# Kernel optimization log

Measured on AMD Instinct MI355X. Metric: run time of the kernel, lower is better.

## Reference

```python
import jax, jax.numpy as jnp
import numpy as np

D_MODEL = 1024
NUM_HEADS = 16
HEAD_DIM = D_MODEL // NUM_HEADS


def setup_inputs() -> dict:
    key = jax.random.key(0)
    ks = jax.random.split(key, 9)
    s = 1.0 / np.sqrt(D_MODEL)
    x = jax.random.normal(ks[0], (2, 2048, D_MODEL), dtype=jnp.float32)
    Wq = jax.random.normal(ks[1], (D_MODEL, D_MODEL), dtype=jnp.float32) * s
    Wk = jax.random.normal(ks[2], (D_MODEL, D_MODEL), dtype=jnp.float32) * s
    Wv = jax.random.normal(ks[3], (D_MODEL, D_MODEL), dtype=jnp.float32) * s
    Wo = jax.random.normal(ks[4], (D_MODEL, D_MODEL), dtype=jnp.float32) * s
    bq = jax.random.normal(ks[5], (D_MODEL,), dtype=jnp.float32) * s
    bk = jax.random.normal(ks[6], (D_MODEL,), dtype=jnp.float32) * s
    bv = jax.random.normal(ks[7], (D_MODEL,), dtype=jnp.float32) * s
    bo = jax.random.normal(ks[8], (D_MODEL,), dtype=jnp.float32) * s
    return {"x": x, "Wq": Wq, "bq": bq, "Wk": Wk, "bk": bk, "Wv": Wv, "bv": bv, "Wo": Wo, "bo": bo}


def reference(x, Wq, bq, Wk, bk, Wv, bv, Wo, bo):
    B, S, D = x.shape
    H, Hd = NUM_HEADS, HEAD_DIM
    # QKV projections
    q = (x @ Wq + bq).reshape(B, S, H, Hd).transpose(0, 2, 1, 3)  # [B,H,S,Hd]
    k = (x @ Wk + bk).reshape(B, S, H, Hd).transpose(0, 2, 1, 3)
    v = (x @ Wv + bv).reshape(B, S, H, Hd).transpose(0, 2, 1, 3)
    scores = jnp.einsum("bhqd,bhkd->bhqk", q, k) / jnp.sqrt(jnp.float32(Hd))
    attn = jax.nn.softmax(scores, axis=-1)
    out = jnp.einsum("bhqk,bhkd->bhqd", attn, v)  # [B,H,S,Hd]
    out = out.transpose(0, 2, 1, 3).reshape(B, S, D)
    return out @ Wo + bo
```

## Files before the change

kernel.cpp:

```cpp
#include <hip/hip_runtime.h>
#include <hip/hip_bf16.h>


typedef unsigned short u16;

#define D_MODEL 1024
#define NHEAD 16
#define HDIM 64
#define BATCH 2
#define SEQ 2048
#define MTOT (BATCH * SEQ)

#define QSCALE 0.18033688011112042f

using frag_ab = __attribute__((ext_vector_type(8))) short;
using frag_cd = __attribute__((ext_vector_type(4))) float;

__device__ __forceinline__ u16 f2u(float f) {
    union { float f; unsigned int i; } x;
    x.f = f;
    unsigned int r = x.i + 0x7fffu + ((x.i >> 16) & 1u);
    return (u16)(r >> 16);
}
__device__ __forceinline__ u16 f2u_fast(float f) {
    union { float f; unsigned int i; } x;
    x.f = f;
    return (u16)((x.i + 0x8000u) >> 16);
}

__global__ void prep(const float* __restrict__ W0, const float* __restrict__ W1,
                     const float* __restrict__ W2, const float* __restrict__ W3,
                     const float* __restrict__ X, u16* __restrict__ Wt,
                     u16* __restrict__ Xb) {
    const int z = blockIdx.z;
    const int tx = threadIdx.x, ty = threadIdx.y;
    if (z < 4) {
        __shared__ u16 t[32][33];
        const float* W = (z == 0) ? W0 : (z == 1) ? W1 : (z == 2) ? W2 : W3;
        u16* o = Wt + (size_t)z * D_MODEL * D_MODEL;
        int n0 = blockIdx.x * 32, k0 = blockIdx.y * 32;
        #pragma unroll
        for (int i = ty; i < 32; i += 8) t[i][tx] = f2u(W[(size_t)(k0 + i) * D_MODEL + n0 + tx]);
        __syncthreads();
        #pragma unroll
        for (int i = ty; i < 32; i += 8) o[(size_t)(n0 + i) * D_MODEL + k0 + tx] = t[tx][i];
    } else {
        int tid = ty * 32 + tx;
        size_t base = ((size_t)(blockIdx.y * 32 + blockIdx.x) * 256 + tid) * 16;
        #pragma unroll
        for (int c = 0; c < 4; ++c) {
            float4 v = *(const float4*)&X[base + c * 4];
            ushort4 o;
            o.x = f2u(v.x); o.y = f2u(v.y); o.z = f2u(v.z); o.w = f2u(v.w);
            *(ushort4*)&Xb[base + c * 4] = o;
        }
    }
}

__launch_bounds__(256, 2)
__global__ void gemm_qkvt(const u16* __restrict__ xb, const u16* __restrict__ Wt,
                          const float* __restrict__ bq, const float* __restrict__ bk,
                          const float* __restrict__ bv, u16* __restrict__ QKw,
                          u16* __restrict__ Vtw) {
    constexpr int BK = 64;
    __shared__ __attribute__((aligned(16))) u16 As[128 * BK];
    __shared__ __attribute__((aligned(16))) u16 Bs[128 * BK];

    const int tid = threadIdx.x;
    const int w = tid >> 6;
    const int lane = tid & 63;
    const int lrow = lane & 15, lquad = lane >> 4;
    const size_t WSZ = (size_t)D_MODEL * D_MODEL;

    const int bid = blockIdx.x;
    const bool vt = bid >= 512;
    const int z = vt ? 2 : (bid >> 8);
    const int t = vt ? (bid - 512) : (bid & 255);
    const int n0 = vt ? (t & 31) * 128 : (t & 7) * 128;
    const int m0 = vt ? (t >> 5) * 128 : (t >> 3) * 128;
    const u16* Ap = vt ? (Wt + 2 * WSZ) : xb;
    const u16* Bp = vt ? xb : (Wt + (size_t)z * WSZ);
    const float* bias = vt ? bv : (z ? bk : bq);

    frag_cd acc[4][4];
    #pragma unroll
    for (int i = 0; i < 4; i++)
        #pragma unroll
        for (int j = 0; j < 4; j++) acc[i][j] = (frag_cd){0.f, 0.f, 0.f, 0.f};

    const int wm = (w >> 1) * 64, wn = (w & 1) * 64;

    for (int k0 = 0; k0 < D_MODEL; k0 += BK) {
        __syncthreads();
        #pragma unroll
        for (int it = 0; it < 4; ++it) {
            int c = it * 256 + tid;
            int r = c >> 3, c8 = c & 7;
            const u16* ga = Ap + (size_t)(m0 + r) * D_MODEL + k0 + c8 * 8;
            char* la = (char*)As + (it * 256 + w * 64) * 16;
            __builtin_amdgcn_global_load_lds((const __attribute__((address_space(1))) void*)ga,
                                             (__attribute__((address_space(3))) void*)la, 16, 0, 0);
            const u16* gb = Bp + (size_t)(n0 + r) * D_MODEL + k0 + c8 * 8;
            char* lb = (char*)Bs + (it * 256 + w * 64) * 16;
            __builtin_amdgcn_global_load_lds((const __attribute__((address_space(1))) void*)gb,
                                             (__attribute__((address_space(3))) void*)lb, 16, 0, 0);
        }
        __syncthreads();

        #pragma unroll
        for (int kc = 0; kc < 2; ++kc) {
            frag_ab av[4], bvv[4];
            #pragma unroll
            for (int i = 0; i < 4; i++)
                av[i] = *(const frag_ab*)&As[(wm + i * 16 + lrow) * BK + kc * 32 + lquad * 8];
            #pragma unroll
            for (int j = 0; j < 4; j++)
                bvv[j] = *(const frag_ab*)&Bs[(wn + j * 16 + lrow) * BK + kc * 32 + lquad * 8];
            #pragma unroll
            for (int i = 0; i < 4; i++)
                #pragma unroll
                for (int j = 0; j < 4; j++)
                    acc[i][j] = __builtin_amdgcn_mfma_f32_16x16x32_bf16(av[i], bvv[j], acc[i][j], 0, 0, 0);
        }
    }

    const float scale = (!vt && z == 0) ? QSCALE : 1.0f;
    #pragma unroll
    for (int j = 0; j < 4; j++) {
        int gn = n0 + wn + j * 16 + lrow;
        #pragma unroll
        for (int i = 0; i < 4; i++) {
            #pragma unroll
            for (int rr = 0; rr < 4; ++rr) {
                int gm = m0 + wm + i * 16 + lquad * 4 + rr;
                if (!vt) {
                    float v = (acc[i][j][rr] + bias[gn]) * scale;
                    u16* oz = QKw + (size_t)z * ((size_t)MTOT * D_MODEL);
                    int b = gm >> 11, s = gm & (SEQ - 1);
                    int h = gn >> 6, d = gn & (HDIM - 1);
                    oz[(((size_t)(b * NHEAD + h)) * SEQ + s) * HDIM + d] = f2u(v);
                } else {
                    float v = acc[i][j][rr] + bias[gm];
                    int h = gm >> 6, d = gm & (HDIM - 1);
                    int b = gn >> 11, s = gn & (SEQ - 1);
                    Vtw[(((size_t)(b * NHEAD + h)) * HDIM + d) * SEQ + s] = f2u(v);
                }
            }
        }
    }
}

__launch_bounds__(256, 2)
__global__ void gemm_out(const u16* __restrict__ A, const u16* __restrict__ Wt,
                         const float* __restrict__ bias, float* __restrict__ out) {
    constexpr int BK = 64;
    __shared__ __attribute__((aligned(16))) u16 As[64 * BK];
    __shared__ __attribute__((aligned(16))) u16 Bs[128 * BK];

    const int tid = threadIdx.x;
    const int w = tid >> 6;
    const int lane = tid & 63;
    const int lrow = lane & 15, lquad = lane >> 4;
    const int m0 = blockIdx.y * 64, n0 = blockIdx.x * 128;

    frag_cd acc[2][4];
    #pragma unroll
    for (int i = 0; i < 2; i++)
        #pragma unroll
        for (int j = 0; j < 4; j++) acc[i][j] = (frag_cd){0.f, 0.f, 0.f, 0.f};

    const int wm = (w >> 1) * 32, wn = (w & 1) * 64;

    for (int k0 = 0; k0 < D_MODEL; k0 += BK) {
        __syncthreads();
        #pragma unroll
        for (int it = 0; it < 2; ++it) {
            int c = it * 256 + tid;
            int r = c >> 3, c8 = c & 7;
            const u16* ga = A + (size_t)(m0 + r) * D_MODEL + k0 + c8 * 8;
            char* la = (char*)As + (it * 256 + w * 64) * 16;
            __builtin_amdgcn_global_load_lds((const __attribute__((address_space(1))) void*)ga,
                                             (__attribute__((address_space(3))) void*)la, 16, 0, 0);
        }
        #pragma unroll
        for (int it = 0; it < 4; ++it) {
            int c = it * 256 + tid;
            int r = c >> 3, c8 = c & 7;
            const u16* gb = Wt + (size_t)(n0 + r) * D_MODEL + k0 + c8 * 8;
            char* lb = (char*)Bs + (it * 256 + w * 64) * 16;
            __builtin_amdgcn_global_load_lds((const __attribute__((address_space(1))) void*)gb,
                                             (__attribute__((address_space(3))) void*)lb, 16, 0, 0);
        }
        __syncthreads();

        #pragma unroll
        for (int kc = 0; kc < 2; ++kc) {
            frag_ab av[2], bvv[4];
            #pragma unroll
            for (int i = 0; i < 2; i++)
                av[i] = *(const frag_ab*)&As[(wm + i * 16 + lrow) * BK + kc * 32 + lquad * 8];
            #pragma unroll
            for (int j = 0; j < 4; j++)
                bvv[j] = *(const frag_ab*)&Bs[(wn + j * 16 + lrow) * BK + kc * 32 + lquad * 8];
            #pragma unroll
            for (int i = 0; i < 2; i++)
                #pragma unroll
                for (int j = 0; j < 4; j++)
                    acc[i][j] = __builtin_amdgcn_mfma_f32_16x16x32_bf16(av[i], bvv[j], acc[i][j], 0, 0, 0);
        }
    }

    #pragma unroll
    for (int j = 0; j < 4; j++) {
        int gn = n0 + wn + j * 16 + lrow;
        float bvf = bias[gn];
        #pragma unroll
        for (int i = 0; i < 2; i++)
            #pragma unroll
            for (int rr = 0; rr < 4; ++rr) {
                int gm = m0 + wm + i * 16 + lquad * 4 + rr;
                out[(size_t)gm * D_MODEL + gn] = acc[i][j][rr] + bvf;
            }
    }
}

__launch_bounds__(256, 2)
__global__ void attn_kernel(const u16* __restrict__ Q, const u16* __restrict__ K,
                            const u16* __restrict__ Vt, u16* __restrict__ O) {
    constexpr int SKK = 72;
    constexpr int SKV = 136;
    __shared__ __attribute__((aligned(16))) u16 Ks[128 * SKK];
    __shared__ __attribute__((aligned(16))) u16 Vs[64 * SKV];
    __shared__ __attribute__((aligned(16))) u16 Ps[4 * 32 * SKV];

    const int tid = threadIdx.x;
    const int w = tid >> 6;
    const int lane = tid & 63;
    const int lrow = lane & 15, lquad = lane >> 4;
    const int bh = blockIdx.y;
    const int q0 = blockIdx.x * 128;
    const size_t base = (size_t)bh * SEQ * HDIM;
    const u16* Qg = Q + base;
    const u16* Kg = K + base;
    const u16* Vg = Vt + base;

    frag_ab qf[2][2];
    #pragma unroll
    for (int sub = 0; sub < 2; ++sub)
        #pragma unroll
        for (int kc = 0; kc < 2; ++kc)
            qf[sub][kc] = *(const frag_ab*)&Qg[(size_t)(q0 + w * 32 + sub * 16 + lrow) * HDIM + kc * 32 + lquad * 8];

    frag_cd accO[2][4], lacc[2];
    #pragma unroll
    for (int sub = 0; sub < 2; ++sub) {
        lacc[sub] = (frag_cd){0.f, 0.f, 0.f, 0.f};
        #pragma unroll
        for (int df = 0; df < 4; df++) accO[sub][df] = (frag_cd){0.f, 0.f, 0.f, 0.f};
    }
    frag_ab ones;
    #pragma unroll
    for (int t = 0; t < 8; ++t) ones[t] = (short)0x3F80;

    u16* Pw = Ps + w * 32 * SKV;

    for (int kt = 0; kt < SEQ / 128; ++kt) {
        __syncthreads();
        #pragma unroll
        for (int it = 0; it < 4; ++it) {
            int c = it * 256 + tid;
            int rk = c >> 3, ck = (c & 7) * 8;
            *(uint4*)&Ks[rk * SKK + ck] = *(const uint4*)&Kg[(size_t)(kt * 128 + rk) * HDIM + ck];
            int rv = c >> 4, cv = (c & 15) * 8;
            *(uint4*)&Vs[rv * SKV + cv] = *(const uint4*)&Vg[(size_t)rv * SEQ + kt * 128 + cv];
        }
        __syncthreads();

        frag_cd sc[2][8];
        #pragma unroll
        for (int sub = 0; sub < 2; ++sub)
            #pragma unroll
            for (int nf = 0; nf < 8; nf++) sc[sub][nf] = (frag_cd){0.f, 0.f, 0.f, 0.f};
        #pragma unroll
        for (int kc = 0; kc < 2; ++kc) {
            #pragma unroll
            for (int nf = 0; nf < 8; nf++) {
                frag_ab kf = *(const frag_ab*)&Ks[(nf * 16 + lrow) * SKK + kc * 32 + lquad * 8];
                #pragma unroll
                for (int sub = 0; sub < 2; ++sub)
                    sc[sub][nf] = __builtin_amdgcn_mfma_f32_16x16x32_bf16(qf[sub][kc], kf, sc[sub][nf], 0, 0, 0);
            }
        }

        #pragma unroll
        for (int sub = 0; sub < 2; ++sub)
            #pragma unroll
            for (int nf = 0; nf < 8; nf++)
                #pragma unroll
                for (int i = 0; i < 4; i++)
                    Pw[(sub * 16 + lquad * 4 + i) * SKV + nf * 16 + lrow] = f2u_fast(exp2f(sc[sub][nf][i]));

        #pragma unroll
        for (int kc = 0; kc < 4; ++kc) {
            frag_ab pf[2];
            #pragma unroll
            for (int sub = 0; sub < 2; ++sub)
                pf[sub] = *(const frag_ab*)&Pw[(sub * 16 + lrow) * SKV + kc * 32 + lquad * 8];
            #pragma unroll
            for (int sub = 0; sub < 2; ++sub)
                lacc[sub] = __builtin_amdgcn_mfma_f32_16x16x32_bf16(pf[sub], ones, lacc[sub], 0, 0, 0);
            #pragma unroll
            for (int df = 0; df < 4; df++) {
                frag_ab vf = *(const frag_ab*)&Vs[(df * 16 + lrow) * SKV + kc * 32 + lquad * 8];
                #pragma unroll
                for (int sub = 0; sub < 2; ++sub)
                    accO[sub][df] = __builtin_amdgcn_mfma_f32_16x16x32_bf16(pf[sub], vf, accO[sub][df], 0, 0, 0);
            }
        }
    }

    const int b = bh >> 4, h = bh & (NHEAD - 1);
    #pragma unroll
    for (int sub = 0; sub < 2; ++sub)
        #pragma unroll
        for (int df = 0; df < 4; df++)
            #pragma unroll
            for (int i = 0; i < 4; i++) {
                int s = q0 + w * 32 + sub * 16 + lquad * 4 + i;
                int d = df * 16 + lrow;
                O[((size_t)(b * SEQ + s)) * D_MODEL + h * HDIM + d] = f2u(accO[sub][df][i] / lacc[sub][i]);
            }
}

extern "C" void kernel_launch(void* const* d_in, const int* in_sizes, int n_in,
                              void* d_out, int out_size, void* d_ws, size_t ws_size,
                              hipStream_t stream) {
    const float* x  = (const float*)d_in[0];
    const float* Wq = (const float*)d_in[1];
    const float* bq = (const float*)d_in[2];
    const float* Wk = (const float*)d_in[3];
    const float* bk = (const float*)d_in[4];
    const float* Wv = (const float*)d_in[5];
    const float* bv = (const float*)d_in[6];
    const float* Wo = (const float*)d_in[7];
    const float* bo = (const float*)d_in[8];

    u16* ws = (u16*)d_ws;
    const size_t WSZ = (size_t)D_MODEL * D_MODEL;
    const size_t TSZ = (size_t)MTOT * D_MODEL;
    u16* xb  = ws;
    u16* Wt  = ws + 4 * WSZ;
    u16* QKw = ws + 8 * WSZ;
    u16* Vtw = QKw + 2 * TSZ;
    u16* Aw  = Vtw + TSZ;

    prep<<<dim3(32, 32, 5), dim3(32, 8), 0, stream>>>(Wq, Wk, Wv, Wo, x, Wt, xb);
    gemm_qkvt<<<dim3(768), 256, 0, stream>>>(xb, Wt, bq, bk, bv, QKw, Vtw);
    attn_kernel<<<dim3(16, 32), 256, 0, stream>>>(QKw, QKw + TSZ, Vtw, Aw);
    gemm_out<<<dim3(8, 64), 256, 0, stream>>>(Aw, Wt + 3 * WSZ, bo, (float*)d_out);
}
```

Before: 223.6 us.

## Use 8 waves of 16 query rows each in attention and raise occupancy bounds

The attention kernel moves from 4 waves each handling 32 query rows to 8 waves each handling 16 rows, with 512 threads per block. This halves per-wave register state and spreads the cooperative K/V tile loads across more threads. The intent is more latency hiding through higher occupancy. The cost is that each K and V fragment read from shared memory now feeds half as many MFMAs, adding LDS traffic per unit of work. The QKV GEMM's launch bound is also raised to 3 blocks per CU, which may force register spills.

```diff
diff --git a/kernel.cpp b/kernel.cpp
--- a/kernel.cpp
+++ b/kernel.cpp
@@ -57,7 +57,7 @@
     }
 }
 
-__launch_bounds__(256, 2)
+__launch_bounds__(256, 3)
 __global__ void gemm_qkvt(const u16* __restrict__ xb, const u16* __restrict__ Wt,
                           const float* __restrict__ bq, const float* __restrict__ bk,
                           const float* __restrict__ bv, u16* __restrict__ QKw,
@@ -224,14 +224,14 @@
     }
 }
 
-__launch_bounds__(256, 2)
+__launch_bounds__(512, 4)
 __global__ void attn_kernel(const u16* __restrict__ Q, const u16* __restrict__ K,
                             const u16* __restrict__ Vt, u16* __restrict__ O) {
     constexpr int SKK = 72;
     constexpr int SKV = 136;
     __shared__ __attribute__((aligned(16))) u16 Ks[128 * SKK];
     __shared__ __attribute__((aligned(16))) u16 Vs[64 * SKV];
-    __shared__ __attribute__((aligned(16))) u16 Ps[4 * 32 * SKV];
+    __shared__ __attribute__((aligned(16))) u16 Ps[8 * 16 * SKV];
 
     const int tid = threadIdx.x;
     const int w = tid >> 6;
@@ -244,31 +244,26 @@
     const u16* Kg = K + base;
     const u16* Vg = Vt + base;
 
-    frag_ab qf[2][2];
-    #pragma unroll
-    for (int sub = 0; sub < 2; ++sub)
-        #pragma unroll
-        for (int kc = 0; kc < 2; ++kc)
-            qf[sub][kc] = *(const frag_ab*)&Qg[(size_t)(q0 + w * 32 + sub * 16 + lrow) * HDIM + kc * 32 + lquad * 8];
-
-    frag_cd accO[2][4], lacc[2];
-    #pragma unroll
-    for (int sub = 0; sub < 2; ++sub) {
-        lacc[sub] = (frag_cd){0.f, 0.f, 0.f, 0.f};
-        #pragma unroll
-        for (int df = 0; df < 4; df++) accO[sub][df] = (frag_cd){0.f, 0.f, 0.f, 0.f};
-    }
+    frag_ab qf[2];
+    #pragma unroll
+    for (int kc = 0; kc < 2; ++kc)
+        qf[kc] = *(const frag_ab*)&Qg[(size_t)(q0 + w * 16 + lrow) * HDIM + kc * 32 + lquad * 8];
+
+    frag_cd accO[4], lacc;
+    lacc = (frag_cd){0.f, 0.f, 0.f, 0.f};
+    #pragma unroll
+    for (int df = 0; df < 4; df++) accO[df] = (frag_cd){0.f, 0.f, 0.f, 0.f};
     frag_ab ones;
     #pragma unroll
     for (int t = 0; t < 8; ++t) ones[t] = (short)0x3F80;
 
-    u16* Pw = Ps + w * 32 * SKV;
+    u16* Pw = Ps + w * 16 * SKV;
 
     for (int kt = 0; kt < SEQ / 128; ++kt) {
         __syncthreads();
         #pragma unroll
-        for (int it = 0; it < 4; ++it) {
-            int c = it * 256 + tid;
+        for (int it = 0; it < 2; ++it) {
+            int c = it * 512 + tid;
             int rk = c >> 3, ck = (c & 7) * 8;
             *(uint4*)&Ks[rk * SKK + ck] = *(const uint4*)&Kg[(size_t)(kt * 128 + rk) * HDIM + ck];
             int rv = c >> 4, cv = (c & 15) * 8;
@@ -276,60 +271,45 @@
         }
         __syncthreads();
 
-        frag_cd sc[2][8];
-        #pragma unroll
-        for (int sub = 0; sub < 2; ++sub)
-            #pragma unroll
-            for (int nf = 0; nf < 8; nf++) sc[sub][nf] = (frag_cd){0.f, 0.f, 0.f, 0.f};
+        frag_cd sc[8];
+        #pragma unroll
+        for (int nf = 0; nf < 8; nf++) sc[nf] = (frag_cd){0.f, 0.f, 0.f, 0.f};
         #pragma unroll
         for (int kc = 0; kc < 2; ++kc) {
             #pragma unroll
             for (int nf = 0; nf < 8; nf++) {
                 frag_ab kf = *(const frag_ab*)&Ks[(nf * 16 + lrow) * SKK + kc * 32 + lquad * 8];
-                #pragma unroll
-                for (int sub = 0; sub < 2; ++sub)
-                    sc[sub][nf] = __builtin_amdgcn_mfma_f32_16x16x32_bf16(qf[sub][kc], kf, sc[sub][nf], 0, 0, 0);
+                sc[nf] = __builtin_amdgcn_mfma_f32_16x16x32_bf16(qf[kc], kf, sc[nf], 0, 0, 0);
             }
         }
 
         #pragma unroll
-        for (int sub = 0; sub < 2; ++sub)
-            #pragma unroll
-            for (int nf = 0; nf < 8; nf++)
-                #pragma unroll
-                for (int i = 0; i < 4; i++)
-                    Pw[(sub * 16 + lquad * 4 + i) * SKV + nf * 16 + lrow] = f2u_fast(exp2f(sc[sub][nf][i]));
+        for (int nf = 0; nf < 8; nf++)
+            #pragma unroll
+            for (int i = 0; i < 4; i++)
+                Pw[(lquad * 4 + i) * SKV + nf * 16 + lrow] = f2u_fast(exp2f(sc[nf][i]));
 
         #pragma unroll
         for (int kc = 0; kc < 4; ++kc) {
-            frag_ab pf[2];
-            #pragma unroll
-            for (int sub = 0; sub < 2; ++sub)
-                pf[sub] = *(const frag_ab*)&Pw[(sub * 16 + lrow) * SKV + kc * 32 + lquad * 8];
-            #pragma unroll
-            for (int sub = 0; sub < 2; ++sub)
-                lacc[sub] = __builtin_amdgcn_mfma_f32_16x16x32_bf16(pf[sub], ones, lacc[sub], 0, 0, 0);
+            frag_ab pf = *(const frag_ab*)&Pw[lrow * SKV + kc * 32 + lquad * 8];
+            lacc = __builtin_amdgcn_mfma_f32_16x16x32_bf16(pf, ones, lacc, 0, 0, 0);
             #pragma unroll
             for (int df = 0; df < 4; df++) {
                 frag_ab vf = *(const frag_ab*)&Vs[(df * 16 + lrow) * SKV + kc * 32 + lquad * 8];
-                #pragma unroll
-                for (int sub = 0; sub < 2; ++sub)
-                    accO[sub][df] = __builtin_amdgcn_mfma_f32_16x16x32_bf16(pf[sub], vf, accO[sub][df], 0, 0, 0);
+                accO[df] = __builtin_amdgcn_mfma_f32_16x16x32_bf16(pf, vf, accO[df], 0, 0, 0);
             }
         }
     }
 
     const int b = bh >> 4, h = bh & (NHEAD - 1);
     #pragma unroll
-    for (int sub = 0; sub < 2; ++sub)
-        #pragma unroll
-        for (int df = 0; df < 4; df++)
-            #pragma unroll
-            for (int i = 0; i < 4; i++) {
-                int s = q0 + w * 32 + sub * 16 + lquad * 4 + i;
-                int d = df * 16 + lrow;
-                O[((size_t)(b * SEQ + s)) * D_MODEL + h * HDIM + d] = f2u(accO[sub][df][i] / lacc[sub][i]);
-            }
+    for (int df = 0; df < 4; df++)
+        #pragma unroll
+        for (int i = 0; i < 4; i++) {
+            int s = q0 + w * 16 + lquad * 4 + i;
+            int d = df * 16 + lrow;
+            O[((size_t)(b * SEQ + s)) * D_MODEL + h * HDIM + d] = f2u(accO[df][i] / lacc[i]);
+        }
 }
 
 extern "C" void kernel_launch(void* const* d_in, const int* in_sizes, int n_in,
@@ -356,6 +336,6 @@
 
     prep<<<dim3(32, 32, 5), dim3(32, 8), 0, stream>>>(Wq, Wk, Wv, Wo, x, Wt, xb);
     gemm_qkvt<<<dim3(768), 256, 0, stream>>>(xb, Wt, bq, bk, bv, QKw, Vtw);
-    attn_kernel<<<dim3(16, 32), 256, 0, stream>>>(QKw, QKw + TSZ, Vtw, Aw);
+    attn_kernel<<<dim3(16, 32), 512, 0, stream>>>(QKw, QKw + TSZ, Vtw, Aw);
     gemm_out<<<dim3(8, 64), 256, 0, stream>>>(Aw, Wt + 3 * WSZ, bo, (float*)d_out);
 }
```

Result: no change. 223.1 us (-0.2%).
